# Performance work log

Measured on AMD Instinct MI355X. Metric: run time of the kernel, lower is better.

The kernel has to match this reference:

```python
import jax, jax.numpy as jnp
import numpy as np

K_TOP = 2  # top-k experts per token


def setup_inputs() -> dict:
    key = jax.random.key(0)
    k1, k2, k3 = jax.random.split(key, 3)
    B, S, H, E = 4, 2048, 1024, 8
    hidden_states = jax.random.normal(k1, (B, S, H), dtype=jnp.float32)
    router_w = jax.random.normal(k2, (E, H), dtype=jnp.float32) * 0.02
    expert_weights = jax.random.normal(k3, (E, H, H), dtype=jnp.float32) * 0.02
    return {"hidden_states": hidden_states, "router_w": router_w, "expert_weights": expert_weights}


def reference(hidden_states, router_w, expert_weights):
    B, S, H = hidden_states.shape
    x = hidden_states.reshape(-1, H)                      # [N, H], N = B*S
    logits = x @ router_w.T                               # [N, E]
    probs = jax.nn.softmax(logits, axis=-1)               # [N, E]
    topk_vals, topk_idx = jax.lax.top_k(probs, K_TOP)     # [N, K]
    topk_w = topk_vals / (topk_vals.sum(-1, keepdims=True) + 1e-6)  # [N, K]

    # Dense per-expert GEMM over all tokens (single-device dispatch = identity)
    expert_out = jnp.einsum('nh,eho->eno', x, expert_weights)  # [E, N, H]

    # all_to_all_combine: gather each token's K expert outputs
    combined = jnp.take_along_axis(
        expert_out.transpose(1, 0, 2),                    # [N, E, H]
        topk_idx[:, :, None], axis=1)                     # [N, K, H]
    combined = combined.transpose(1, 0, 2)                # [K, N, H]

    # remap bias: sum over last dim of one-hot(topk_idx) * router_prob == gathered prob
    remap_bias = jnp.take_along_axis(probs, topk_idx, axis=1).T[:, :, None]  # [K, N, 1]

    weights = topk_w.T[:, :, None]                        # [K, N, 1]
    out = ((combined + remap_bias) * weights).sum(axis=0) # [N, H]
    return out.reshape(B, S, H)
```

## Files before the change

kernel.cpp:

```cpp
#include <hip/hip_runtime.h>
#include <hip/hip_fp16.h>
#include <cstdint>

typedef unsigned short u16;
typedef __attribute__((ext_vector_type(8))) short short8;
typedef __attribute__((ext_vector_type(4))) float float4v;

#define NTOK 8192
#define HDIM 1024
#define NEXP 8
#define TM 128
#define TN 128
#define BK 32
#define NITER (HDIM / BK)
#define LA_N (TM * BK)
#define LB_N (TN * BK)
#define MAXT 136
#define WBLK 2048
#define RBLK 2048

__device__ __forceinline__ u16 f2bf(float f) {
    union { float f; uint32_t u; } v; v.f = f;
    uint32_t u = v.u;
    return (u16)((u + 0x7FFFu + ((u >> 16) & 1u)) >> 16);
}

__device__ __forceinline__ void gll16(const u16* g, u16* l) {
    __builtin_amdgcn_global_load_lds(
        (const __attribute__((address_space(1))) uint32_t*)g,
        (__attribute__((address_space(3))) uint32_t*)l,
        16, 0, 0);
}

__global__ __launch_bounds__(256) void prep(const float* __restrict__ x,
                                            const float* __restrict__ rw,
                                            const float* __restrict__ ew,
                                            u16* __restrict__ x_bf,
                                            u16* __restrict__ w_bf,
                                            float* __restrict__ wt0,
                                            float* __restrict__ wt1,
                                            float* __restrict__ biasv,
                                            int* __restrict__ sel,
                                            int* __restrict__ ctrl) {
    if (blockIdx.x == 0 && threadIdx.x < 132) ctrl[threadIdx.x] = 0;

    if (blockIdx.x < WBLK) {
        __shared__ float tile[64][65];
        const int bid = blockIdx.x;
        const int e  = bid >> 8;
        const int k0 = ((bid >> 4) & 15) * 64;
        const int n0 = (bid & 15) * 64;
        const int kr = threadIdx.x >> 2;
        const int ng = (threadIdx.x & 3) * 16;
        const float* src = ew + ((size_t)e << 20) + (size_t)(k0 + kr) * HDIM + n0 + ng;
#pragma unroll
        for (int j = 0; j < 4; j++) {
            const float4 v = *(const float4*)(src + 4 * j);
            tile[kr][ng + 4*j]     = v.x;
            tile[kr][ng + 4*j + 1] = v.y;
            tile[kr][ng + 4*j + 2] = v.z;
            tile[kr][ng + 4*j + 3] = v.w;
        }
        __syncthreads();
        const int nr = threadIdx.x >> 2;
        const int kg = (threadIdx.x & 3) * 16;
        u16* dst = w_bf + ((size_t)e << 20) + (size_t)(n0 + nr) * HDIM + k0 + kg;
#pragma unroll
        for (int j = 0; j < 4; j++) {
            ushort4 o;
            o.x = f2bf(tile[kg + 4*j][nr]);
            o.y = f2bf(tile[kg + 4*j + 1][nr]);
            o.z = f2bf(tile[kg + 4*j + 2][nr]);
            o.w = f2bf(tile[kg + 4*j + 3][nr]);
            *(ushort4*)(dst + 4 * j) = o;
        }
    } else {
        const int wv = threadIdx.x >> 6;
        const int l  = threadIdx.x & 63;
        const int n  = (blockIdx.x - WBLK) * 4 + wv;
        const float4* xr = (const float4*)(x + (size_t)n * HDIM);
        ushort4* xo = (ushort4*)(x_bf + (size_t)n * HDIM);

        float4 xv[4];
#pragma unroll
        for (int t = 0; t < 4; t++) {
            xv[t] = xr[t * 64 + l];
            ushort4 p;
            p.x = f2bf(xv[t].x); p.y = f2bf(xv[t].y);
            p.z = f2bf(xv[t].z); p.w = f2bf(xv[t].w);
            xo[t * 64 + l] = p;
        }

        float logits[NEXP];
#pragma unroll
        for (int e = 0; e < NEXP; e++) {
            const float4* rwe = (const float4*)(rw + e * HDIM);
            float acc = 0.f;
#pragma unroll
            for (int t = 0; t < 4; t++) {
                const float4 r = rwe[t * 64 + l];
                acc += xv[t].x * r.x + xv[t].y * r.y + xv[t].z * r.z + xv[t].w * r.w;
            }
#pragma unroll
            for (int s = 32; s > 0; s >>= 1) acc += __shfl_xor(acc, s, 64);
            logits[e] = acc;
        }

        if (l == 0) {
            float mx = logits[0];
#pragma unroll
            for (int e = 1; e < NEXP; e++) mx = fmaxf(mx, logits[e]);
            float p[NEXP]; float sum = 0.f;
#pragma unroll
            for (int e = 0; e < NEXP; e++) { p[e] = expf(logits[e] - mx); sum += p[e]; }
            const float inv = 1.f / sum;
#pragma unroll
            for (int e = 0; e < NEXP; e++) p[e] *= inv;
            int e0 = 0;
#pragma unroll
            for (int e = 1; e < NEXP; e++) if (p[e] > p[e0]) e0 = e;
            int e1 = (e0 == 0) ? 1 : 0;
#pragma unroll
            for (int e = 0; e < NEXP; e++) if (e != e0 && p[e] > p[e1]) e1 = e;
            const float p0 = p[e0], p1 = p[e1];
            const float wsum = p0 + p1 + 1e-6f;
            const float w0 = p0 / wsum, w1 = p1 / wsum;
            wt0[n] = w0; wt1[n] = w1;
            biasv[n] = w0 * p0 + w1 * p1;
            sel[n] = e0 | (e1 << 8);
        }
    }
}

__global__ __launch_bounds__(256) void build_lists(const int* __restrict__ sel,
                                                   int* __restrict__ lists,
                                                   int* __restrict__ ctrl,
                                                   int* __restrict__ tmap) {
    const int n  = blockIdx.x * 256 + threadIdx.x;
    const int wv = threadIdx.x >> 6;
    const int l  = threadIdx.x & 63;
    const int s  = sel[n];
    const int e0 = s & 0xFF, e1 = s >> 8;
    __shared__ int wcnt[NEXP][4];
    __shared__ int ebase[NEXP];
    int pf0 = 0, pf1 = 0;
    const unsigned long long ltmask = (1ULL << l) - 1ULL;
#pragma unroll
    for (int e = 0; e < NEXP; e++) {
        const int slot = (e0 == e) ? 0 : ((e1 == e) ? 1 : -1);
        const unsigned long long bal = __ballot(slot >= 0);
        const int pf = __popcll(bal & ltmask);
        if (slot == 0) pf0 = pf;
        if (slot == 1) pf1 = pf;
        if (l == 0) wcnt[e][wv] = __popcll(bal);
    }
    __syncthreads();
    if (threadIdx.x < NEXP) {
        const int e = threadIdx.x;
        const int tot = wcnt[e][0] + wcnt[e][1] + wcnt[e][2] + wcnt[e][3];
        ebase[e] = atomicAdd(&ctrl[e * 16], tot);
    }
    __syncthreads();
    int off0 = ebase[e0], off1 = ebase[e1];
#pragma unroll
    for (int i = 0; i < 4; i++) {
        off0 += (i < wv) ? wcnt[e0][i] : 0;
        off1 += (i < wv) ? wcnt[e1][i] : 0;
    }
    lists[e0 * NTOK + off0 + pf0] = n;
    lists[e1 * NTOK + off1 + pf1] = n | 0x10000;

    __shared__ int lastflag;
    __threadfence();
    if (threadIdx.x == 0) lastflag = (atomicAdd(&ctrl[128], 1) == (int)gridDim.x - 1);
    __syncthreads();
    if (lastflag) {
        __shared__ int tbase[NEXP + 1];
        if (threadIdx.x == 0) {
            int acc = 0;
            for (int e = 0; e < NEXP; e++) {
                tbase[e] = acc;
                acc += (atomicAdd(&ctrl[e * 16], 0) + TM - 1) / TM;
            }
            tbase[NEXP] = acc;
        }
        __syncthreads();
        for (int i = threadIdx.x; i < MAXT; i += 256) {
            int v = -1;
#pragma unroll
            for (int e = 0; e < NEXP; e++)
                if (i >= tbase[e] && i < tbase[e + 1]) v = (e << 16) | (i - tbase[e]);
            tmap[i] = v;
        }
    }
}

__global__ __launch_bounds__(256, 3) void moe_gemm(const u16* __restrict__ x_bf,
                                                   const u16* __restrict__ wt_bf,
                                                   const int* __restrict__ lists,
                                                   const int* __restrict__ ctrl,
                                                   const int* __restrict__ tmap,
                                                   const float* __restrict__ wt0,
                                                   const float* __restrict__ wt1,
                                                   const float* __restrict__ biasv,
                                                   __half* __restrict__ stage0,
                                                   __half* __restrict__ stage1) {
    const int ent = tmap[blockIdx.x];
    if (ent < 0) return;
    const int e = ent >> 16;
    const int tile_m = (ent & 0xFFFF) * TM;
    const int cnt = ctrl[e * 16];
    const int tn = blockIdx.y * TN;

    __shared__ u16 lA[3 * LA_N];
    __shared__ u16 lB[3 * LB_N];
    __shared__ int   toks[TM];
    __shared__ float wgt[TM];
    __shared__ float bia[TM];
    __shared__ int   slt[TM];

    const int t  = threadIdx.x;
    const int wv = t >> 6;
    const int l  = t & 63;

    if (t < TM) {
        const int idx = tile_m + t;
        int tok = 0; float w = 0.f, b = 0.f; int sl = 0;
        if (idx < cnt) {
            const int entry = lists[e * NTOK + idx];
            tok = entry & 0xFFFF;
            sl = entry >> 16;
            w = sl ? wt1[tok] : wt0[tok];
            b = sl ? 0.f : biasv[tok];
        }
        toks[t] = tok; wgt[t] = w; bia[t] = b; slt[t] = sl;
    }
    __syncthreads();

    const u16* gA[2]; const u16* gB[2]; int dAB[2];
#pragma unroll
    for (int i = 0; i < 2; i++) {
        const int slot = (i * 4 + wv) * 64 + l;
        const int row  = slot >> 2;
        const int c    = (slot & 3) ^ ((row >> 1) & 3);
        gA[i] = x_bf + (size_t)toks[row] * HDIM + c * 8;
        gB[i] = wt_bf + ((size_t)e << 20) + (size_t)(tn + row) * HDIM + c * 8;
        dAB[i] = (i * 4 + wv) * 512;
    }

    const int wm = (wv & 1) * 64;
    const int wn = (wv >> 1) * 64;
    const int fm = l & 15;
    const int fq = l >> 4;
    int aoff[4], boff[4];
#pragma unroll
    for (int i = 0; i < 4; i++) {
        const int ra = wm + i * 16 + fm;
        const int rb = wn + i * 16 + fm;
        aoff[i] = ra * BK + ((fq ^ ((ra >> 1) & 3)) * 8);
        boff[i] = rb * BK + ((fq ^ ((rb >> 1) & 3)) * 8);
    }

    float4v acc[4][4];
#pragma unroll
    for (int i = 0; i < 4; i++)
#pragma unroll
        for (int j = 0; j < 4; j++) { float4v z = {0.f, 0.f, 0.f, 0.f}; acc[i][j] = z; }

    short8 afr[2][4], bfr[2][4];

#pragma unroll
    for (int tk = 0; tk < 3; tk++) {
#pragma unroll
        for (int i = 0; i < 2; i++) {
            gll16(gA[i] + tk * BK, lA + tk * LA_N + dAB[i]);
            gll16(gB[i] + tk * BK, lB + tk * LB_N + dAB[i]);
        }
    }
    asm volatile("s_waitcnt vmcnt(8)\n\ts_barrier" ::: "memory");
#pragma unroll
    for (int i = 0; i < 4; i++) {
        afr[0][i] = *(const short8*)&lA[aoff[i]];
        bfr[0][i] = *(const short8*)&lB[boff[i]];
    }

#pragma unroll
    for (int it = 0; it < NITER; ++it) {
        const int cs = it & 1;
        const int ns = cs ^ 1;

        if (it == 0) {
            asm volatile("s_waitcnt vmcnt(4)\n\ts_barrier" ::: "memory");
        } else if (it < NITER - 1) {
            asm volatile("s_waitcnt vmcnt(0)\n\ts_barrier" ::: "memory");
        }

        if (it >= 1 && it + 2 < NITER) {
            const int nb = (it + 2) % 3;
            const int nk = (it + 2) * BK;
#pragma unroll
            for (int i = 0; i < 2; i++) {
                gll16(gA[i] + nk, lA + nb * LA_N + dAB[i]);
                gll16(gB[i] + nk, lB + nb * LB_N + dAB[i]);
            }
        }

        if (it + 1 < NITER) {
            const u16* ca = lA + ((it + 1) % 3) * LA_N;
            const u16* cb = lB + ((it + 1) % 3) * LB_N;
#pragma unroll
            for (int i = 0; i < 4; i++) {
                afr[ns][i] = *(const short8*)&ca[aoff[i]];
                bfr[ns][i] = *(const short8*)&cb[boff[i]];
            }
            asm volatile("s_waitcnt lgkmcnt(8)" ::: "memory");
        } else {
            asm volatile("s_waitcnt lgkmcnt(0)" ::: "memory");
        }
        __builtin_amdgcn_sched_barrier(0);

        __builtin_amdgcn_s_setprio(1);
#pragma unroll
        for (int i = 0; i < 4; i++)
#pragma unroll
            for (int nf = 0; nf < 4; nf++)
                acc[i][nf] = __builtin_amdgcn_mfma_f32_16x16x32_bf16(
                    afr[cs][i], bfr[cs][nf], acc[i][nf], 0, 0, 0);
        __builtin_amdgcn_s_setprio(0);
    }

#pragma unroll
    for (int mf = 0; mf < 4; mf++) {
#pragma unroll
        for (int r = 0; r < 4; r++) {
            const int m_local = wm + mf * 16 + fq * 4 + r;
            if (tile_m + m_local < cnt) {
                const int tok = toks[m_local];
                const float w = wgt[m_local], b = bia[m_local];
                __half* sp = (slt[m_local] ? stage1 : stage0) + (size_t)tok * HDIM;
#pragma unroll
                for (int nf = 0; nf < 4; nf++) {
                    const int h = tn + wn + nf * 16 + fm;
                    sp[h] = __float2half(acc[mf][nf][r] * w + b);
                }
            }
        }
    }
}

__global__ __launch_bounds__(256) void combine(const __half* __restrict__ s0,
                                               const __half* __restrict__ s1,
                                               float* __restrict__ out) {
    const size_t idx = ((size_t)blockIdx.x * 256 + threadIdx.x) * 8;
    union { uint4 v; __half h[8]; } a, b;
    a.v = *(const uint4*)(s0 + idx);
    b.v = *(const uint4*)(s1 + idx);
    float4 o0, o1;
    o0.x = __half2float(a.h[0]) + __half2float(b.h[0]);
    o0.y = __half2float(a.h[1]) + __half2float(b.h[1]);
    o0.z = __half2float(a.h[2]) + __half2float(b.h[2]);
    o0.w = __half2float(a.h[3]) + __half2float(b.h[3]);
    o1.x = __half2float(a.h[4]) + __half2float(b.h[4]);
    o1.y = __half2float(a.h[5]) + __half2float(b.h[5]);
    o1.z = __half2float(a.h[6]) + __half2float(b.h[6]);
    o1.w = __half2float(a.h[7]) + __half2float(b.h[7]);
    *(float4*)(out + idx)     = o0;
    *(float4*)(out + idx + 4) = o1;
}

extern "C" void kernel_launch(void* const* d_in, const int* in_sizes, int n_in,
                              void* d_out, int out_size, void* d_ws, size_t ws_size,
                              hipStream_t stream) {
    const float* x  = (const float*)d_in[0];
    const float* rw = (const float*)d_in[1];
    const float* ew = (const float*)d_in[2];
    float* out = (float*)d_out;

    char* ws = (char*)d_ws;
    u16*    x_bf   = (u16*)ws;
    u16*    w_bf   = (u16*)(ws + 16777216);
    __half* stage0 = (__half*)(ws + 33554432);
    __half* stage1 = (__half*)(ws + 50331648);
    float*  wt0    = (float*)(ws + 67108864);
    float*  wt1    = (float*)(ws + 67141632);
    float*  biasv  = (float*)(ws + 67174400);
    int*    sel    = (int*)(ws + 67207168);
    int*    lists  = (int*)(ws + 67239936);
    int*    ctrl   = (int*)(ws + 67502080);
    int*    tmap   = (int*)(ws + 67502720);

    prep<<<WBLK + RBLK, 256, 0, stream>>>(x, rw, ew, x_bf, w_bf, wt0, wt1, biasv, sel, ctrl);
    build_lists<<<NTOK / 256, 256, 0, stream>>>(sel, lists, ctrl, tmap);
    moe_gemm<<<dim3(MAXT, HDIM / TN, 1), 256, 0, stream>>>(
        x_bf, w_bf, lists, ctrl, tmap, wt0, wt1, biasv, stage0, stage1);
    combine<<<(NTOK * HDIM) / (256 * 8), 256, 0, stream>>>(stage0, stage1, out);
}
```

Baseline: 195.1 us.

## Switch GEMM to double-buffered LDS and single fragment set for higher occupancy

Replaces the triple-buffered LDS pipeline with register-double-buffered fragments by a simpler two-stage LDS double buffer, loading fragments from the current stage each iteration. Launch bounds rise from 3 to 4 blocks per CU. The goal is to cut LDS and register use so more waves can hide latency. The cost is a shallower prefetch distance and a full vmcnt/lgkmcnt wait every iteration, which exposes LDS read latency before the MFMAs.

```diff
diff --git a/kernel.cpp b/kernel.cpp
--- a/kernel.cpp
+++ b/kernel.cpp
@@ -195,7 +195,7 @@
     }
 }
 
-__global__ __launch_bounds__(256, 3) void moe_gemm(const u16* __restrict__ x_bf,
+__global__ __launch_bounds__(256, 4) void moe_gemm(const u16* __restrict__ x_bf,
                                                    const u16* __restrict__ wt_bf,
                                                    const int* __restrict__ lists,
                                                    const int* __restrict__ ctrl,
@@ -212,8 +212,8 @@
     const int cnt = ctrl[e * 16];
     const int tn = blockIdx.y * TN;
 
-    __shared__ u16 lA[3 * LA_N];
-    __shared__ u16 lB[3 * LB_N];
+    __shared__ u16 lA[2 * LA_N];
+    __shared__ u16 lB[2 * LB_N];
     __shared__ int   toks[TM];
     __shared__ float wgt[TM];
     __shared__ float bia[TM];
@@ -267,37 +267,19 @@
 #pragma unroll
         for (int j = 0; j < 4; j++) { float4v z = {0.f, 0.f, 0.f, 0.f}; acc[i][j] = z; }
 
-    short8 afr[2][4], bfr[2][4];
-
-#pragma unroll
-    for (int tk = 0; tk < 3; tk++) {
-#pragma unroll
-        for (int i = 0; i < 2; i++) {
-            gll16(gA[i] + tk * BK, lA + tk * LA_N + dAB[i]);
-            gll16(gB[i] + tk * BK, lB + tk * LB_N + dAB[i]);
-        }
-    }
-    asm volatile("s_waitcnt vmcnt(8)\n\ts_barrier" ::: "memory");
-#pragma unroll
-    for (int i = 0; i < 4; i++) {
-        afr[0][i] = *(const short8*)&lA[aoff[i]];
-        bfr[0][i] = *(const short8*)&lB[boff[i]];
+#pragma unroll
+    for (int i = 0; i < 2; i++) {
+        gll16(gA[i], lA + dAB[i]);
+        gll16(gB[i], lB + dAB[i]);
     }
 
 #pragma unroll
     for (int it = 0; it < NITER; ++it) {
-        const int cs = it & 1;
-        const int ns = cs ^ 1;
-
-        if (it == 0) {
-            asm volatile("s_waitcnt vmcnt(4)\n\ts_barrier" ::: "memory");
-        } else if (it < NITER - 1) {
-            asm volatile("s_waitcnt vmcnt(0)\n\ts_barrier" ::: "memory");
-        }
-
-        if (it >= 1 && it + 2 < NITER) {
-            const int nb = (it + 2) % 3;
-            const int nk = (it + 2) * BK;
+        asm volatile("s_waitcnt vmcnt(0)\n\ts_barrier" ::: "memory");
+
+        if (it + 1 < NITER) {
+            const int nb = (it + 1) & 1;
+            const int nk = (it + 1) * BK;
 #pragma unroll
             for (int i = 0; i < 2; i++) {
                 gll16(gA[i] + nk, lA + nb * LA_N + dAB[i]);
@@ -305,18 +287,15 @@
             }
         }
 
-        if (it + 1 < NITER) {
-            const u16* ca = lA + ((it + 1) % 3) * LA_N;
-            const u16* cb = lB + ((it + 1) % 3) * LB_N;
-#pragma unroll
-            for (int i = 0; i < 4; i++) {
-                afr[ns][i] = *(const short8*)&ca[aoff[i]];
-                bfr[ns][i] = *(const short8*)&cb[boff[i]];
-            }
-            asm volatile("s_waitcnt lgkmcnt(8)" ::: "memory");
-        } else {
-            asm volatile("s_waitcnt lgkmcnt(0)" ::: "memory");
-        }
+        const u16* ca = lA + (it & 1) * LA_N;
+        const u16* cb = lB + (it & 1) * LB_N;
+        short8 afr[4], bfr[4];
+#pragma unroll
+        for (int i = 0; i < 4; i++) {
+            afr[i] = *(const short8*)&ca[aoff[i]];
+            bfr[i] = *(const short8*)&cb[boff[i]];
+        }
+        asm volatile("s_waitcnt lgkmcnt(0)" ::: "memory");
         __builtin_amdgcn_sched_barrier(0);
 
         __builtin_amdgcn_s_setprio(1);
@@ -325,7 +304,7 @@
 #pragma unroll
             for (int nf = 0; nf < 4; nf++)
                 acc[i][nf] = __builtin_amdgcn_mfma_f32_16x16x32_bf16(
-                    afr[cs][i], bfr[cs][nf], acc[i][nf], 0, 0, 0);
+                    afr[i], bfr[nf], acc[i][nf], 0, 0, 0);
         __builtin_amdgcn_s_setprio(0);
     }
 
```

Measured after the change: 197.0 us. No clear change (+1.0%).
